# Kernel tuning notes

Measured on AMD Instinct MI355X. Metric: run time of the kernel, lower is better.

The kernel has to match this reference:

```python
import jax, jax.numpy as jnp
import numpy as np

ACT_BIT = 8
W_BIT = 8
EPS = 1e-8


def ste_round(x):
    # straight-through round (matches torch STE quant autograd)
    return x + jax.lax.stop_gradient(jnp.round(x) - x)


def quant_act(x):
    """Per-tensor symmetric 8-bit activation quantization (HAWQ QuantAct)."""
    n = 2 ** (ACT_BIT - 1) - 1  # 127
    x_max = jax.lax.stop_gradient(jnp.max(jnp.abs(x)))
    scale = jnp.maximum(x_max, EPS) / n
    x_int = jnp.clip(ste_round(x / scale), -n - 1, n)
    return x_int * scale, scale


def quant_linear(x_q, act_scale, weight, bias):
    """Per-channel symmetric 8-bit weight quant + integer matmul + fused dequant."""
    n = 2 ** (W_BIT - 1) - 1  # 127
    w_max = jax.lax.stop_gradient(jnp.max(jnp.abs(weight), axis=1, keepdims=True))  # [out,1]
    w_scale = jnp.maximum(w_max, EPS) / n                                            # [out,1]
    w_int = jnp.clip(ste_round(weight / w_scale), -n - 1, n)                         # [out,in]
    bias_scale = w_scale[:, 0] * act_scale                                           # [out]
    b_int = ste_round(bias / bias_scale)                                             # [out]
    x_int = x_q / act_scale                                   # integer-valued float, [..., in]
    out_int = jnp.einsum('...i,oi->...o', x_int, w_int)       # int8-domain GEMM in float
    return (out_int + b_int) * bias_scale                     # fused dequant


def setup_inputs() -> dict:
    key = jax.random.key(0)
    k1, k2, k3 = jax.random.split(key, 3)
    L, B, Q, D, O = 6, 8, 1024, 1024, 1024
    hs = jax.random.normal(k1, (L, B, Q, D), dtype=jnp.float32)
    weight = jax.random.normal(k2, (O, D), dtype=jnp.float32) * 0.02
    bias = jax.random.normal(k3, (O,), dtype=jnp.float32) * 0.02
    return {"hs": hs, "weight": weight, "bias": bias}


def reference(hs, weight, bias):
    x_q, act_scale = quant_act(hs)
    return quant_linear(x_q, act_scale, weight, bias)
```

## Files before the change

kernel.cpp:

```cpp
#include <hip/hip_runtime.h>
#include <stdint.h>

typedef int i32x4 __attribute__((ext_vector_type(4)));

#define K_DIM 1024
#define BM 256
#define BN 256
#define BKK 64
#define NKT (K_DIM / BKK)


__device__ __forceinline__ int quant1(float v, float inv) {
  float t = rintf(v * inv);
  t = fminf(fmaxf(t, -128.0f), 127.0f);
  return (int)t;
}

__device__ __forceinline__ void gld_lds16(const signed char* g, signed char* l) {
  typedef const __attribute__((address_space(1))) unsigned int* gp_t;
  typedef __attribute__((address_space(3))) unsigned int* lp_t;
  __builtin_amdgcn_global_load_lds((gp_t)(const void*)g, (lp_t)(void*)l, 16, 0, 0);
}

__global__ void absmax_kernel(const float* __restrict__ x, unsigned int* __restrict__ amax,
                              long long n4) {
  long long i = (long long)blockIdx.x * blockDim.x + threadIdx.x;
  const long long stride = (long long)gridDim.x * blockDim.x;
  const float4* x4 = (const float4*)x;
  float m = 0.0f;
  for (; i < n4; i += stride) {
    float4 v = x4[i];
    m = fmaxf(m, fmaxf(fmaxf(fabsf(v.x), fabsf(v.y)), fmaxf(fabsf(v.z), fabsf(v.w))));
  }
#pragma unroll
  for (int off = 32; off > 0; off >>= 1) m = fmaxf(m, __shfl_down(m, off, 64));
  __shared__ float sm[4];
  const int lane = threadIdx.x & 63, wid = threadIdx.x >> 6;
  if (lane == 0) sm[wid] = m;
  __syncthreads();
  if (threadIdx.x == 0) {
    float b = fmaxf(fmaxf(sm[0], sm[1]), fmaxf(sm[2], sm[3]));
    atomicMax(amax, __float_as_uint(b));
  }
}

__global__ void wquant_kernel(const float* __restrict__ w, const float* __restrict__ bias,
                              const unsigned int* __restrict__ amax_u,
                              signed char* __restrict__ wq,
                              float* __restrict__ bscale, float* __restrict__ bint) {
  const int o = blockIdx.x;
  const int t = threadIdx.x;
  float4 v = ((const float4*)(w + (size_t)o * K_DIM))[t];
  float m = fmaxf(fmaxf(fabsf(v.x), fabsf(v.y)), fmaxf(fabsf(v.z), fabsf(v.w)));
#pragma unroll
  for (int off = 32; off > 0; off >>= 1) m = fmaxf(m, __shfl_down(m, off, 64));
  __shared__ float sm[4];
  __shared__ float s_scale;
  const int lane = t & 63, wid = t >> 6;
  if (lane == 0) sm[wid] = m;
  __syncthreads();
  if (t == 0) {
    float wm = fmaxf(fmaxf(sm[0], sm[1]), fmaxf(sm[2], sm[3]));
    float wsc = fmaxf(wm, 1e-8f) / 127.0f;
    float asc = fmaxf(__uint_as_float(*amax_u), 1e-8f) / 127.0f;
    float bsc = wsc * asc;
    bscale[o] = bsc;
    bint[o] = rintf(bias[o] / bsc);
    s_scale = wsc;
  }
  __syncthreads();
  const float inv = 1.0f / s_scale;
  int q0 = quant1(v.x, inv), q1 = quant1(v.y, inv), q2 = quant1(v.z, inv), q3 = quant1(v.w, inv);
  unsigned int p = (unsigned)(q0 & 255) | ((unsigned)(q1 & 255) << 8) |
                   ((unsigned)(q2 & 255) << 16) | ((unsigned)(q3 & 255) << 24);
  const int F = o >> 4, T = t >> 4;
  const int l = (((t >> 2) & 3) << 4) | (o & 15);
  const int j = (t << 2) & 15;
  *(unsigned int*)(wq + (((size_t)F << 14) + (T << 10) + (l << 4) + j)) = p;
}

__global__ void aquant_kernel(const float* __restrict__ x, const unsigned int* __restrict__ amax_u,
                              uint4* __restrict__ q16, int nchunk) {
  const float asc = fmaxf(__uint_as_float(*amax_u), 1e-8f) / 127.0f;
  const float inv = 1.0f / asc;
  int c = blockIdx.x * blockDim.x + threadIdx.x;
  const int stride = gridDim.x * blockDim.x;
  for (; c < nchunk; c += stride) {
    const int l = c & 63, T = (c >> 6) & 15, F = c >> 10;
    const size_t src = (((size_t)(F << 4) + (l & 15)) << 10) + (T << 6) + ((l >> 4) << 4);
    const float4* s4 = (const float4*)(x + src);
    unsigned int r[4];
#pragma unroll
    for (int q = 0; q < 4; q++) {
      float4 v = s4[q];
      int q0 = quant1(v.x, inv), q1 = quant1(v.y, inv), q2 = quant1(v.z, inv), q3 = quant1(v.w, inv);
      r[q] = (unsigned)(q0 & 255) | ((unsigned)(q1 & 255) << 8) |
             ((unsigned)(q2 & 255) << 16) | ((unsigned)(q3 & 255) << 24);
    }
    q16[c] = make_uint4(r[0], r[1], r[2], r[3]);
  }
}

__global__ __launch_bounds__(512, 2) void gemm_kernel(
    const signed char* __restrict__ A, const signed char* __restrict__ W,
    const float* __restrict__ bscale, const float* __restrict__ bint,
    float* __restrict__ out, int M, int N, int K) {
  extern __shared__ __align__(16) signed char smem[];
  signed char* Abase = smem;
  signed char* Bbase = smem + 65536;

  const int nwg = gridDim.x;
  const int orig = blockIdx.x;
  const int wgid = (orig & 7) * (nwg >> 3) + (orig >> 3);
  const int nbn = N / BN;
  const int bm = wgid / nbn;
  const int bn = wgid % nbn;
  const int m0 = bm * BM, n0 = bn * BN;

  const int tid = threadIdx.x;
  const int lane = tid & 63;
  const int wid = tid >> 6;
  const int wr = wid >> 2;
  const int wc = wid & 3;

  const signed char* gaf = A + (((size_t)(m0 >> 4) + wid) << 14) + (lane << 4);
  const signed char* gbf = W + (((size_t)(n0 >> 4) + wid) << 14) + (lane << 4);
  const size_t fs8 = (size_t)8 << 14;

  i32x4 acc[8][4];
#pragma unroll
  for (int i = 0; i < 8; i++)
#pragma unroll
    for (int j = 0; j < 4; j++) acc[i][j] = (i32x4){0, 0, 0, 0};

  i32x4 af[8], bf[4];

#define SB __builtin_amdgcn_sched_barrier(0)
#define BAR __builtin_amdgcn_s_barrier()
#define WAIT_LGKM0 asm volatile("s_waitcnt lgkmcnt(0)" ::: "memory")

#define ISSUE_TILE(t)                                                     \
  do {                                                                    \
    const int b_ = (t) & 3;                                               \
    const int kof_ = (t) << 10;                                           \
    gld_lds16(gaf + kof_,       Abase + ((b_ * 16 + wid) << 10));         \
    gld_lds16(gaf + fs8 + kof_, Abase + ((b_ * 16 + wid + 8) << 10));     \
    gld_lds16(gbf + kof_,       Bbase + ((b_ * 16 + wid) << 10));         \
    gld_lds16(gbf + fs8 + kof_, Bbase + ((b_ * 16 + wid + 8) << 10));     \
  } while (0)

#define RD_A(i_, mf_) af[i_] = *(const i32x4*)(Abase + (((buf_ * 16) + (mf_)) << 10) + lane * 16)
#define RD_B(j_, nf_) bf[j_] = *(const i32x4*)(Bbase + (((buf_ * 16) + (nf_)) << 10) + lane * 16)

#define MFMA16(IB)                                                             \
  do {                                                                         \
    __builtin_amdgcn_s_setprio(1);                                             \
    _Pragma("unroll") for (int i_ = 0; i_ < 4; i_++)                           \
      _Pragma("unroll") for (int j_ = 0; j_ < 4; j_++)                         \
        acc[(IB) + i_][j_] = __builtin_amdgcn_mfma_i32_16x16x64_i8(            \
            af[(IB) + i_], bf[j_], acc[(IB) + i_][j_], 0, 0, 0);               \
    __builtin_amdgcn_s_setprio(0);                                             \
  } while (0)

#define TILE(t, DO_ISSUE, VMW, DO_VM)                                          \
  do {                                                                         \
    const int buf_ = (t) & 3;                                                  \
    if (DO_ISSUE) ISSUE_TILE((t) + 3);                                         \
    RD_A(0, wr * 8 + 0); RD_A(1, wr * 8 + 1);                                  \
    RD_A(2, wr * 8 + 2); RD_A(3, wr * 8 + 3);                                  \
    RD_B(0, wc * 4 + 0); RD_B(1, wc * 4 + 1);                                  \
    RD_B(2, wc * 4 + 2); RD_B(3, wc * 4 + 3);                                  \
    RD_A(4, wr * 8 + 4); RD_A(5, wr * 8 + 5);                                  \
    RD_A(6, wr * 8 + 6); RD_A(7, wr * 8 + 7);                                  \
    MFMA16(0);                                                                 \
    MFMA16(4);                                                                 \
    if (DO_VM) { asm volatile("s_waitcnt " VMW ::: "memory"); }                \
    SB; BAR; SB;                                                               \
  } while (0)

  ISSUE_TILE(0);
  ISSUE_TILE(1);
  ISSUE_TILE(2);
  asm volatile("s_waitcnt vmcnt(8)" ::: "memory");
  SB; BAR; SB;

#pragma unroll 1
  for (int t = 0; t < NKT - 3; ++t) {
    TILE(t, 1, "vmcnt(8)", 1);
  }
  TILE(NKT - 3, 0, "vmcnt(4)", 1);
  TILE(NKT - 2, 0, "vmcnt(0)", 1);
  TILE(NKT - 1, 0, "", 0);

#undef TILE
#undef MFMA16
#undef RD_A
#undef RD_B
#undef ISSUE_TILE

  float* Cst = (float*)smem;
  const int rr = (lane >> 4) * 4;
  const int cc = lane & 15;
#pragma unroll
  for (int h = 0; h < 2; ++h) {
    if (wr == h) {
#pragma unroll
      for (int j = 0; j < 4; j++) {
        const int colL = wc * 64 + j * 16 + cc;
        const float bs = bscale[n0 + colL];
        const float bi = bint[n0 + colL];
#pragma unroll
        for (int i = 0; i < 8; i++)
#pragma unroll
          for (int r = 0; r < 4; r++)
            Cst[(i * 16 + rr + r) * 256 + colL] = ((float)acc[i][j][r] + bi) * bs;
      }
    }
    WAIT_LGKM0;
    BAR;
    const size_t rowbase = (size_t)(m0 + h * 128) * N + n0;
#pragma unroll
    for (int it = 0; it < 16; ++it) {
      const int r_ = it * 8 + wid;
      float4 v = *(const float4*)&Cst[r_ * 256 + lane * 4];
      *(float4*)&out[rowbase + (size_t)r_ * N + lane * 4] = v;
    }
    WAIT_LGKM0;
    BAR;
  }
#undef WAIT_LGKM0
#undef BAR
#undef SB
}

extern "C" void kernel_launch(void* const* d_in, const int* in_sizes, int n_in,
                              void* d_out, int out_size, void* d_ws, size_t ws_size,
                              hipStream_t stream) {
  const float* hs = (const float*)d_in[0];
  const float* w = (const float*)d_in[1];
  const float* bias = (const float*)d_in[2];
  float* out = (float*)d_out;

  const long long n = (long long)in_sizes[0];
  const int K = K_DIM;
  const int O = in_sizes[2];
  const int M = (int)(n / K);

  char* ws = (char*)d_ws;
  unsigned int* amax_u = (unsigned int*)ws;
  float* bscale = (float*)(ws + 256);
  float* bint = (float*)(ws + 256 + 4096);
  signed char* wq = (signed char*)(ws + 65536);
  signed char* xq = (signed char*)(ws + 65536 + 1048576);

  hipFuncSetAttribute((const void*)gemm_kernel,
                      hipFuncAttributeMaxDynamicSharedMemorySize, 131072);

  hipMemsetAsync(amax_u, 0, 4, stream);

  const long long n4 = n / 4;
  absmax_kernel<<<2048, 256, 0, stream>>>(hs, amax_u, n4);
  wquant_kernel<<<O, 256, 0, stream>>>(w, bias, amax_u, wq, bscale, bint);
  const int nchunk = (int)(n / 16);
  aquant_kernel<<<2048, 256, 0, stream>>>(hs, amax_u, (uint4*)xq, nchunk);

  const int nblocks = (M / BM) * (O / BN);
  gemm_kernel<<<nblocks, 512, 131072, stream>>>(xq, wq, bscale, bint, out, M, O, K);
}
```

Baseline: 186.4 us.

## Load B fragments directly to registers and halve GEMM LDS footprint

The GEMM now stages only the A tile through LDS. Each wave loads its B fragments straight from global memory into double-buffered registers one k-tile ahead, which cuts dynamic LDS from 128KB to 64KB and reduces LDS read traffic. The epilogue is split into four 64-row passes to fit the smaller LDS, and the K loop is fully unrolled. The atomic absmax plus memset is replaced by a two-stage partial/final reduction; the risks are more register pressure and redundant global reads of B across waves.

```diff
diff --git a/kernel.cpp b/kernel.cpp
--- a/kernel.cpp
+++ b/kernel.cpp
@@ -22,8 +22,12 @@
   __builtin_amdgcn_global_load_lds((gp_t)(const void*)g, (lp_t)(void*)l, 16, 0, 0);
 }
 
-__global__ void absmax_kernel(const float* __restrict__ x, unsigned int* __restrict__ amax,
-                              long long n4) {
+#define SB __builtin_amdgcn_sched_barrier(0)
+#define BAR __builtin_amdgcn_s_barrier()
+#define WAIT_LGKM0 asm volatile("s_waitcnt lgkmcnt(0)" ::: "memory")
+
+__global__ void absmax_part(const float* __restrict__ x, float* __restrict__ parts,
+                            long long n4) {
   long long i = (long long)blockIdx.x * blockDim.x + threadIdx.x;
   const long long stride = (long long)gridDim.x * blockDim.x;
   const float4* x4 = (const float4*)x;
@@ -38,10 +42,23 @@
   const int lane = threadIdx.x & 63, wid = threadIdx.x >> 6;
   if (lane == 0) sm[wid] = m;
   __syncthreads();
-  if (threadIdx.x == 0) {
-    float b = fmaxf(fmaxf(sm[0], sm[1]), fmaxf(sm[2], sm[3]));
-    atomicMax(amax, __float_as_uint(b));
-  }
+  if (threadIdx.x == 0)
+    parts[blockIdx.x] = fmaxf(fmaxf(sm[0], sm[1]), fmaxf(sm[2], sm[3]));
+}
+
+__global__ void absmax_fin(const float* __restrict__ parts, unsigned int* __restrict__ amax_u,
+                           int nparts) {
+  const int t = threadIdx.x;
+  float m = 0.0f;
+  for (int i = t; i < nparts; i += 256) m = fmaxf(m, parts[i]);
+#pragma unroll
+  for (int off = 32; off > 0; off >>= 1) m = fmaxf(m, __shfl_down(m, off, 64));
+  __shared__ float sm[4];
+  const int lane = t & 63, wid = t >> 6;
+  if (lane == 0) sm[wid] = m;
+  __syncthreads();
+  if (t == 0)
+    amax_u[0] = __float_as_uint(fmaxf(fmaxf(sm[0], sm[1]), fmaxf(sm[2], sm[3])));
 }
 
 __global__ void wquant_kernel(const float* __restrict__ w, const float* __restrict__ bias,
@@ -107,7 +124,6 @@
     float* __restrict__ out, int M, int N, int K) {
   extern __shared__ __align__(16) signed char smem[];
   signed char* Abase = smem;
-  signed char* Bbase = smem + 65536;
 
   const int nwg = gridDim.x;
   const int orig = blockIdx.x;
@@ -120,12 +136,12 @@
   const int tid = threadIdx.x;
   const int lane = tid & 63;
   const int wid = tid >> 6;
-  const int wr = wid >> 2;
+  const int wr = wid >> 1 >> 1;
   const int wc = wid & 3;
 
   const signed char* gaf = A + (((size_t)(m0 >> 4) + wid) << 14) + (lane << 4);
-  const signed char* gbf = W + (((size_t)(n0 >> 4) + wid) << 14) + (lane << 4);
   const size_t fs8 = (size_t)8 << 14;
+  const signed char* gbf = W + (((size_t)(n0 >> 4) + wc * 4) << 14) + (lane << 4);
 
   i32x4 acc[8][4];
 #pragma unroll
@@ -133,94 +149,104 @@
 #pragma unroll
     for (int j = 0; j < 4; j++) acc[i][j] = (i32x4){0, 0, 0, 0};
 
-  i32x4 af[8], bf[4];
-
-#define SB __builtin_amdgcn_sched_barrier(0)
-#define BAR __builtin_amdgcn_s_barrier()
-#define WAIT_LGKM0 asm volatile("s_waitcnt lgkmcnt(0)" ::: "memory")
-
-#define ISSUE_TILE(t)                                                     \
-  do {                                                                    \
-    const int b_ = (t) & 3;                                               \
-    const int kof_ = (t) << 10;                                           \
-    gld_lds16(gaf + kof_,       Abase + ((b_ * 16 + wid) << 10));         \
-    gld_lds16(gaf + fs8 + kof_, Abase + ((b_ * 16 + wid + 8) << 10));     \
-    gld_lds16(gbf + kof_,       Bbase + ((b_ * 16 + wid) << 10));         \
-    gld_lds16(gbf + fs8 + kof_, Bbase + ((b_ * 16 + wid + 8) << 10));     \
-  } while (0)
-
-#define RD_A(i_, mf_) af[i_] = *(const i32x4*)(Abase + (((buf_ * 16) + (mf_)) << 10) + lane * 16)
-#define RD_B(j_, nf_) bf[j_] = *(const i32x4*)(Bbase + (((buf_ * 16) + (nf_)) << 10) + lane * 16)
-
-#define MFMA16(IB)                                                             \
+  i32x4 af[8];
+  i32x4 bfA[4], bfB[4];
+
+#define LOADB(L, tt)                                                           \
+  do {                                                                         \
+    L[0] = *(const i32x4*)(gbf + ((size_t)0 << 14) + ((tt) << 10));            \
+    L[1] = *(const i32x4*)(gbf + ((size_t)1 << 14) + ((tt) << 10));            \
+    L[2] = *(const i32x4*)(gbf + ((size_t)2 << 14) + ((tt) << 10));            \
+    L[3] = *(const i32x4*)(gbf + ((size_t)3 << 14) + ((tt) << 10));            \
+  } while (0)
+
+#define ISSUEA(tt)                                                             \
+  do {                                                                         \
+    gld_lds16(gaf + ((size_t)(tt) << 10),                                      \
+              Abase + ((((tt) & 3) * 16 + wid) << 10));                        \
+    gld_lds16(gaf + fs8 + ((size_t)(tt) << 10),                                \
+              Abase + ((((tt) & 3) * 16 + wid + 8) << 10));                    \
+  } while (0)
+
+#define RD_A(t, i_)                                                            \
+  af[i_] = *(const i32x4*)(Abase + ((((t) & 3) * 16 + wr * 8 + (i_)) << 10) + (lane << 4))
+
+#define MFMA16U(IB, U)                                                         \
   do {                                                                         \
     __builtin_amdgcn_s_setprio(1);                                             \
     _Pragma("unroll") for (int i_ = 0; i_ < 4; i_++)                           \
       _Pragma("unroll") for (int j_ = 0; j_ < 4; j_++)                         \
         acc[(IB) + i_][j_] = __builtin_amdgcn_mfma_i32_16x16x64_i8(            \
-            af[(IB) + i_], bf[j_], acc[(IB) + i_][j_], 0, 0, 0);               \
+            af[(IB) + i_], U[j_], acc[(IB) + i_][j_], 0, 0, 0);                \
     __builtin_amdgcn_s_setprio(0);                                             \
   } while (0)
 
-#define TILE(t, DO_ISSUE, VMW, DO_VM)                                          \
-  do {                                                                         \
-    const int buf_ = (t) & 3;                                                  \
-    if (DO_ISSUE) ISSUE_TILE((t) + 3);                                         \
-    RD_A(0, wr * 8 + 0); RD_A(1, wr * 8 + 1);                                  \
-    RD_A(2, wr * 8 + 2); RD_A(3, wr * 8 + 3);                                  \
-    RD_B(0, wc * 4 + 0); RD_B(1, wc * 4 + 1);                                  \
-    RD_B(2, wc * 4 + 2); RD_B(3, wc * 4 + 3);                                  \
-    RD_A(4, wr * 8 + 4); RD_A(5, wr * 8 + 5);                                  \
-    RD_A(6, wr * 8 + 6); RD_A(7, wr * 8 + 7);                                  \
-    MFMA16(0);                                                                 \
-    MFMA16(4);                                                                 \
-    if (DO_VM) { asm volatile("s_waitcnt " VMW ::: "memory"); }                \
+#define TILE(t, U, L, DOB, DOA, VMW, DOVM)                                     \
+  do {                                                                         \
+    if (DOB) LOADB(L, (t) + 1);                                                \
+    if (DOA) ISSUEA((t) + 3);                                                  \
+    SB;                                                                        \
+    RD_A(t, 0); RD_A(t, 1); RD_A(t, 2); RD_A(t, 3);                            \
+    RD_A(t, 4); RD_A(t, 5); RD_A(t, 6); RD_A(t, 7);                            \
+    MFMA16U(0, U);                                                             \
+    MFMA16U(4, U);                                                             \
+    if (DOVM) { asm volatile("s_waitcnt " VMW ::: "memory"); }                 \
     SB; BAR; SB;                                                               \
   } while (0)
 
-  ISSUE_TILE(0);
-  ISSUE_TILE(1);
-  ISSUE_TILE(2);
-  asm volatile("s_waitcnt vmcnt(8)" ::: "memory");
+  ISSUEA(0); ISSUEA(1); ISSUEA(2);
+  LOADB(bfA, 0);
+  asm volatile("s_waitcnt vmcnt(0)" ::: "memory");
   SB; BAR; SB;
 
-#pragma unroll 1
-  for (int t = 0; t < NKT - 3; ++t) {
-    TILE(t, 1, "vmcnt(8)", 1);
-  }
-  TILE(NKT - 3, 0, "vmcnt(4)", 1);
-  TILE(NKT - 2, 0, "vmcnt(0)", 1);
-  TILE(NKT - 1, 0, "", 0);
+  TILE(0,  bfA, bfB, 1, 1, "vmcnt(8)", 1);
+  TILE(1,  bfB, bfA, 1, 1, "vmcnt(8)", 1);
+  TILE(2,  bfA, bfB, 1, 1, "vmcnt(8)", 1);
+  TILE(3,  bfB, bfA, 1, 1, "vmcnt(8)", 1);
+  TILE(4,  bfA, bfB, 1, 1, "vmcnt(8)", 1);
+  TILE(5,  bfB, bfA, 1, 1, "vmcnt(8)", 1);
+  TILE(6,  bfA, bfB, 1, 1, "vmcnt(8)", 1);
+  TILE(7,  bfB, bfA, 1, 1, "vmcnt(8)", 1);
+  TILE(8,  bfA, bfB, 1, 1, "vmcnt(8)", 1);
+  TILE(9,  bfB, bfA, 1, 1, "vmcnt(8)", 1);
+  TILE(10, bfA, bfB, 1, 1, "vmcnt(8)", 1);
+  TILE(11, bfB, bfA, 1, 1, "vmcnt(8)", 1);
+  TILE(12, bfA, bfB, 1, 1, "vmcnt(8)", 1);
+  TILE(13, bfB, bfA, 1, 0, "vmcnt(6)", 1);
+  TILE(14, bfA, bfB, 1, 0, "vmcnt(4)", 1);
+  TILE(15, bfB, bfA, 0, 0, "", 0);
 
 #undef TILE
-#undef MFMA16
+#undef MFMA16U
 #undef RD_A
-#undef RD_B
-#undef ISSUE_TILE
+#undef ISSUEA
+#undef LOADB
 
   float* Cst = (float*)smem;
   const int rr = (lane >> 4) * 4;
   const int cc = lane & 15;
 #pragma unroll
-  for (int h = 0; h < 2; ++h) {
-    if (wr == h) {
+  for (int q = 0; q < 4; ++q) {
+    if (wr == (q >> 1)) {
 #pragma unroll
       for (int j = 0; j < 4; j++) {
         const int colL = wc * 64 + j * 16 + cc;
         const float bs = bscale[n0 + colL];
         const float bi = bint[n0 + colL];
 #pragma unroll
-        for (int i = 0; i < 8; i++)
+        for (int i2 = 0; i2 < 4; i2++) {
+          const int i = (q & 1) * 4 + i2;
 #pragma unroll
           for (int r = 0; r < 4; r++)
-            Cst[(i * 16 + rr + r) * 256 + colL] = ((float)acc[i][j][r] + bi) * bs;
+            Cst[(i2 * 16 + rr + r) * 256 + colL] = ((float)acc[i][j][r] + bi) * bs;
+        }
       }
     }
     WAIT_LGKM0;
     BAR;
-    const size_t rowbase = (size_t)(m0 + h * 128) * N + n0;
-#pragma unroll
-    for (int it = 0; it < 16; ++it) {
+    const size_t rowbase = (size_t)(m0 + q * 64) * N + n0;
+#pragma unroll
+    for (int it = 0; it < 8; ++it) {
       const int r_ = it * 8 + wid;
       float4 v = *(const float4*)&Cst[r_ * 256 + lane * 4];
       *(float4*)&out[rowbase + (size_t)r_ * N + lane * 4] = v;
@@ -228,9 +254,6 @@
     WAIT_LGKM0;
     BAR;
   }
-#undef WAIT_LGKM0
-#undef BAR
-#undef SB
 }
 
 extern "C" void kernel_launch(void* const* d_in, const int* in_sizes, int n_in,
@@ -248,22 +271,22 @@
 
   char* ws = (char*)d_ws;
   unsigned int* amax_u = (unsigned int*)ws;
-  float* bscale = (float*)(ws + 256);
-  float* bint = (float*)(ws + 256 + 4096);
+  float* parts = (float*)(ws + 1024);
+  float* bscale = (float*)(ws + 16384);
+  float* bint = (float*)(ws + 20480);
   signed char* wq = (signed char*)(ws + 65536);
   signed char* xq = (signed char*)(ws + 65536 + 1048576);
 
   hipFuncSetAttribute((const void*)gemm_kernel,
-                      hipFuncAttributeMaxDynamicSharedMemorySize, 131072);
-
-  hipMemsetAsync(amax_u, 0, 4, stream);
+                      hipFuncAttributeMaxDynamicSharedMemorySize, 65536);
 
   const long long n4 = n / 4;
-  absmax_kernel<<<2048, 256, 0, stream>>>(hs, amax_u, n4);
+  absmax_part<<<2048, 256, 0, stream>>>(hs, parts, n4);
+  absmax_fin<<<1, 256, 0, stream>>>(parts, amax_u, 2048);
   wquant_kernel<<<O, 256, 0, stream>>>(w, bias, amax_u, wq, bscale, bint);
   const int nchunk = (int)(n / 16);
   aquant_kernel<<<2048, 256, 0, stream>>>(hs, amax_u, (uint4*)xq, nchunk);
 
   const int nblocks = (M / BM) * (O / BN);
-  gemm_kernel<<<nblocks, 512, 131072, stream>>>(xq, wq, bscale, bint, out, M, O, K);
-}
+  gemm_kernel<<<nblocks, 512, 65536, stream>>>(xq, wq, bscale, bint, out, M, O, K);
+}
```

Result: faster. 180.2 us (-3.3%).
